# Kernel tuning notes

Hardware: AMD Instinct MI355X
Metric: run time of the kernel (lower is better)

Reference implementation:

```python
import jax, jax.numpy as jnp
import numpy as np

B, T, H = 2, 2048, 1024
NH, DK = 16, 64          # num_heads, head_dim (key)
VD, DV = 1024, 64        # value_dim, head_v_dim
LCTX, CD = 512, 768      # context length, cond_token_dim
DW, DA, DG, DVR = 64, 64, 128, 16  # lora ranks: decay, a, gate, v
EPS = DK * 1e-5          # GroupNorm eps = head_dim * norm_eps
LOGW_SCALE = -0.6065306597126334   # -exp(-0.5)

def _tshift(x):
    # token shift: out[t] = x[t-1], out[0] = 0
    return jnp.pad(x, ((0, 0), (1, 0), (0, 0)))[:, :-1]

def _forward(hidden_states, context, v_first, x_r, x_w, x_k, x_v, x_a, x_g,
             k_k, k_a, r_k, W_r, W_k, W_v, W_o, W_cond,
             wA, wB, wb, aA, aB, ab, gA, gB, vA, vB, vb, gn_w, gn_b):
    b, t, _ = hidden_states.shape
    # --- cross-attention context: project then linear-resample to length t (align_corners=True) ---
    ctx = context @ W_cond                                  # [B, Lctx, H]
    L = ctx.shape[1]
    pos = jnp.arange(t) * ((L - 1) / (t - 1))
    lo = jnp.floor(pos).astype(jnp.int32)
    hi = jnp.minimum(lo + 1, L - 1)
    f = (pos - lo)[None, :, None]
    ctx = ctx[:, lo] * (1.0 - f) + ctx[:, hi] * f            # [B, T, H]

    dx = _tshift(hidden_states) - hidden_states
    dc = _tshift(ctx) - ctx
    xr = hidden_states + dx * x_r
    xw = hidden_states + dx * x_w
    xa = hidden_states + dx * x_a
    xg = hidden_states + dx * x_g
    xk = ctx + dc * x_k   # key/value come from the (resampled) context: cross attention
    xv = ctx + dc * x_v

    r = xr @ W_r
    w = LOGW_SCALE * jax.nn.sigmoid(jnp.tanh(xw @ wA) @ wB + wb)   # log decay in (-0.6065, 0)
    k = xk @ W_k
    v = xv @ W_v
    # layer_idx != 0: lerp toward v_first with learned gate
    v = v + jax.nn.sigmoid((xv @ vA) @ vB + vb) * (v_first - v)
    a = jax.nn.sigmoid((xa @ aA) @ aB + ab)                         # in-context learning rate
    g = jax.nn.sigmoid(xg @ gA) @ gB                                 # output gate (no bias)

    kk = (k * k_k).reshape(b, t, NH, DK)
    kk = kk / jnp.maximum(jnp.linalg.norm(kk, axis=-1, keepdims=True), 1e-12)
    k = k * (1.0 + (a - 1.0) * k_a)

    rh = r.reshape(b, t, NH, DK)
    wh = w.reshape(b, t, NH, DK)
    kh = k.reshape(b, t, NH, DK)
    vh = v.reshape(b, t, NH, DV)
    ah = -kk
    bh = kk * a.reshape(b, t, NH, DK)

    # --- RWKV7 generalized delta rule recurrence: S[b,h,i(val),j(key)] ---
    def step(S, inp):
        r_t, w_t, k_t, v_t, a_t, b_t = inp
        sab = jnp.einsum('bhij,bhj,bhk->bhik', S, a_t, b_t)
        S = S * jnp.exp(w_t)[:, :, None, :] + sab + jnp.einsum('bhi,bhj->bhij', v_t, k_t)
        return S, jnp.einsum('bhij,bhj->bhi', S, r_t)

    tr = lambda x: jnp.swapaxes(x, 0, 1)  # [T,B,NH,D]
    S0 = jnp.zeros((b, NH, DV, DK), hidden_states.dtype)
    _, o = jax.lax.scan(step, S0, (tr(rh), tr(wh), tr(kh), tr(vh), tr(ah), tr(bh)))
    o = jnp.swapaxes(o, 0, 1)             # [B,T,NH,DV]

    # GroupNorm(num_groups=NH) over value_dim per token
    mu = o.mean(-1, keepdims=True)
    var = o.var(-1, keepdims=True)
    o = (o - mu) * jax.lax.rsqrt(var + EPS)
    o = o.reshape(b, t, VD) * gn_w + gn_b
    # r_k-weighted direct readout
    o = o + ((rh * kh * r_k).sum(-1, keepdims=True) * vh).reshape(b, t, VD)
    return (o * g) @ W_o

def setup_inputs():
    ki = iter(jax.random.split(jax.random.key(0), 48))
    def nrm(shape, s=1.0):
        return jax.random.normal(next(ki), shape, jnp.float32) * s
    def uni(shape):
        return jax.random.uniform(next(ki), shape, dtype=jnp.float32)
    return {
        'hidden_states': nrm((B, T, H)),
        'context': nrm((B, LCTX, CD)),
        'v_first': nrm((B, T, VD)),
        'x_r': uni((1, 1, H)), 'x_w': uni((1, 1, H)), 'x_k': uni((1, 1, H)),
        'x_v': uni((1, 1, H)), 'x_a': uni((1, 1, H)), 'x_g': uni((1, 1, H)),
        'k_k': jnp.full((H,), 0.85, jnp.float32),
        'k_a': jnp.ones((H,), jnp.float32),
        'r_k': nrm((NH, DK), 0.1),
        'W_r': nrm((H, H), 0.03), 'W_k': nrm((H, H), 0.03),
        'W_v': nrm((H, VD), 0.03), 'W_o': nrm((VD, H), 0.03),
        'W_cond': nrm((CD, H), 0.03),
        'wA': nrm((H, DW), 0.05), 'wB': nrm((DW, H), 0.05), 'wb': nrm((H,), 0.3) - 4.0,
        'aA': nrm((H, DA), 0.05), 'aB': nrm((DA, H), 0.05), 'ab': nrm((H,), 0.1),
        'gA': nrm((H, DG), 0.05), 'gB': nrm((DG, VD), 0.05),
        'vA': nrm((H, DVR), 0.05), 'vB': nrm((DVR, VD), 0.05),
        'vb': jnp.ones((VD,), jnp.float32),
        'gn_w': jnp.ones((VD,), jnp.float32), 'gn_b': jnp.zeros((VD,), jnp.float32),
    }

def reference(hidden_states, context, v_first, x_r, x_w, x_k, x_v, x_a, x_g, k_k, k_a, r_k, W_r, W_k, W_v, W_o, W_cond, wA, wB, wb, aA, aB, ab, gA, gB, vA, vB, vb, gn_w, gn_b):
    return _forward(hidden_states, context, v_first, x_r, x_w, x_k, x_v, x_a, x_g, k_k, k_a, r_k, W_r, W_k, W_v, W_o, W_cond, wA, wB, wb, aA, aB, ab, gA, gB, vA, vB, vb, gn_w, gn_b)
```

## Files before the change

kernel.cpp:

```cpp
#include <hip/hip_runtime.h>
#include <cstddef>
#include <cstdint>

#define T_ 2048
#define H_ 1024
#define NH_ 16
#define LCTX 512
#define NC 64
#define CL 32

typedef __attribute__((ext_vector_type(4))) float f4;
typedef __attribute__((ext_vector_type(4))) unsigned short u16x4;
typedef __attribute__((ext_vector_type(8))) short bf16x8;
typedef __attribute__((ext_vector_type(4))) float f32x4;

#define REP16(X) X(0) X(1) X(2) X(3) X(4) X(5) X(6) X(7) X(8) X(9) X(10) X(11) X(12) X(13) X(14) X(15)
#define REP8(X) X(0) X(1) X(2) X(3) X(4) X(5) X(6) X(7)
#define REP4(X) X(0) X(1) X(2) X(3)

__device__ __forceinline__ float sgm(float x) { return 1.0f / (1.0f + expf(-x)); }
__device__ __forceinline__ f4 f4splat(float v) { f4 r; r.x = v; r.y = v; r.z = v; r.w = v; return r; }
__device__ __forceinline__ float hsum4(f4 v) { return (v.x + v.y) + (v.z + v.w); }

__device__ __forceinline__ float rdlane(float v, int l) {
    return __uint_as_float(__builtin_amdgcn_readlane(__float_as_uint(v), l));
}

__device__ __forceinline__ unsigned short f2bf(float x) {
    unsigned u = __float_as_uint(x);
    u += 0x7FFFu + ((u >> 16) & 1u);
    return (unsigned short)(u >> 16);
}
__device__ __forceinline__ float bf2f(unsigned short h) {
    return __uint_as_float(((unsigned)h) << 16);
}

__device__ __forceinline__ void split1(float x, unsigned short& h, unsigned short& l) {
    unsigned u = __float_as_uint(x);
    h = (unsigned short)(u >> 16);
    float r = x - __uint_as_float(u & 0xFFFF0000u);
    l = (unsigned short)(__float_as_uint(r) >> 16);
}
__device__ __forceinline__ void split4(f4 v, u16x4& h, u16x4& l) {
    unsigned short hh, ll;
    split1(v.x, hh, ll); h.x = hh; l.x = ll;
    split1(v.y, hh, ll); h.y = hh; l.y = ll;
    split1(v.z, hh, ll); h.z = hh; l.z = ll;
    split1(v.w, hh, ll); h.w = hh; l.w = ll;
}

__device__ __forceinline__ size_t toff4(int row, int c4, int kpan) {
    const int j = c4 & 31;
    return ((size_t)(row >> 4) * kpan + (c4 >> 5)) * 512
         + ((j & 15) >> 2) * 128 + (row & 15) * 8 + ((j >> 4) << 2);
}
__device__ __forceinline__ size_t toff1(int row, int k, int kpan) {
    const int j = k & 31;
    return ((size_t)(row >> 4) * kpan + (k >> 5)) * 512
         + ((j & 15) >> 2) * 128 + (row & 15) * 8 + ((j >> 4) << 2) + (j & 3);
}

__device__ __forceinline__ void gload16(const void* g, void* l) {
    __builtin_amdgcn_global_load_lds(
        (const __attribute__((address_space(1))) unsigned int*)g,
        (__attribute__((address_space(3))) unsigned int*)l, 16, 0, 0);
}

struct WSeg { const float* W; unsigned short* Th; unsigned short* Tl;
              int K, N, kpan, tile0, tilesN; };
struct WAll { WSeg s[13]; };

__global__ __launch_bounds__(256) void wtrans_all(WAll all)
{
    const int bid = blockIdx.x;
    int si = 0;
    #pragma unroll
    for (int i = 1; i < 13; ++i) if (bid >= all.s[i].tile0) si = i;
    const WSeg sg = all.s[si];
    const int local = bid - sg.tile0;
    const int k0 = (local / sg.tilesN) * 32;
    const int n0 = (local % sg.tilesN) * 32;

    __shared__ float tile[32][33];
    const int t = threadIdx.x;
    const int r = t >> 3, c4 = (t & 7) * 4;
    f4 v = f4splat(0.0f);
    if (k0 + r < sg.K && n0 + c4 < sg.N)
        v = *(const f4*)(sg.W + (size_t)(k0 + r) * sg.N + n0 + c4);
    tile[r][c4 + 0] = v.x; tile[r][c4 + 1] = v.y;
    tile[r][c4 + 2] = v.z; tile[r][c4 + 3] = v.w;
    __syncthreads();
    {
        const int n = n0 + r;
        float x0 = tile[c4 + 0][r], x1 = tile[c4 + 1][r];
        float x2 = tile[c4 + 2][r], x3 = tile[c4 + 3][r];
        u16x4 hv, lv;
        hv.x = f2bf(x0); lv.x = f2bf(x0 - bf2f(hv.x));
        hv.y = f2bf(x1); lv.y = f2bf(x1 - bf2f(hv.y));
        hv.z = f2bf(x2); lv.z = f2bf(x2 - bf2f(hv.z));
        hv.w = f2bf(x3); lv.w = f2bf(x3 - bf2f(hv.w));
        const size_t off = toff4(n, k0 + c4, sg.kpan);
        *(u16x4*)(sg.Th + off) = hv;
        *(u16x4*)(sg.Tl + off) = lv;
    }
}

__global__ __launch_bounds__(256) void ctx_split(
    const float* __restrict__ X, unsigned short* __restrict__ H,
    unsigned short* __restrict__ L)
{
    const int gid = blockIdx.x * 256 + threadIdx.x;
    const int row = gid / 192;
    const int c4 = (gid - row * 192) * 4;
    f4 v = *(const f4*)(X + (size_t)row * 768 + c4);
    u16x4 h, l; split4(v, h, l);
    const size_t off = toff4(row, c4, 24);
    *(u16x4*)(H + off) = h; *(u16x4*)(L + off) = l;
}

__global__ __launch_bounds__(256) void hs_lerp4(
    const float* __restrict__ hs,
    const float* __restrict__ x_r, const float* __restrict__ x_w,
    const float* __restrict__ x_a, const float* __restrict__ x_g,
    unsigned short* __restrict__ xr_h, unsigned short* __restrict__ xr_l,
    unsigned short* __restrict__ xw_h, unsigned short* __restrict__ xw_l,
    unsigned short* __restrict__ xa_h, unsigned short* __restrict__ xa_l,
    unsigned short* __restrict__ xg_h, unsigned short* __restrict__ xg_l)
{
    const int gid = blockIdx.x * 256 + threadIdx.x;
    const int c4 = (gid & 255) * 4;
    const int row = gid >> 8;
    const int tt = row & (T_ - 1);
    const f4 cur = *(const f4*)(hs + (size_t)row * H_ + c4);
    f4 prev = f4splat(0.0f);
    if (tt) prev = *(const f4*)(hs + (size_t)(row - 1) * H_ + c4);
    const f4 d = prev - cur;
    const size_t off = toff4(row, c4, 32);
    u16x4 h, l;
    split4(cur + d * (*(const f4*)(x_r + c4)), h, l);
    *(u16x4*)(xr_h + off) = h; *(u16x4*)(xr_l + off) = l;
    split4(cur + d * (*(const f4*)(x_w + c4)), h, l);
    *(u16x4*)(xw_h + off) = h; *(u16x4*)(xw_l + off) = l;
    split4(cur + d * (*(const f4*)(x_a + c4)), h, l);
    *(u16x4*)(xa_h + off) = h; *(u16x4*)(xa_l + off) = l;
    split4(cur + d * (*(const f4*)(x_g + c4)), h, l);
    *(u16x4*)(xg_h + off) = h; *(u16x4*)(xg_l + off) = l;
}

__device__ __forceinline__ f4 ctx_sample(const float* __restrict__ cp, int b, int t, int c4) {
    const float scale = (float)(511.0 / 2047.0);
    float tf = (float)t * scale;
    int lo = (int)tf;
    float f = tf - (float)lo;
    int hi = lo + 1; if (hi > LCTX - 1) hi = LCTX - 1;
    f4 cl = *(const f4*)(cp + (size_t)(b * LCTX + lo) * 1024 + c4);
    f4 ch = *(const f4*)(cp + (size_t)(b * LCTX + hi) * 1024 + c4);
    return cl + (ch - cl) * f;
}

__global__ __launch_bounds__(256) void ctx_lerp2(
    const float* __restrict__ cp,
    const float* __restrict__ x_k, const float* __restrict__ x_v,
    unsigned short* __restrict__ xk_h, unsigned short* __restrict__ xk_l,
    unsigned short* __restrict__ xv_h, unsigned short* __restrict__ xv_l)
{
    const int gid = blockIdx.x * 256 + threadIdx.x;
    const int c4 = (gid & 255) * 4;
    const int row = gid >> 8;
    const int b = row >> 11;
    const int tt = row & (T_ - 1);
    const f4 cur = ctx_sample(cp, b, tt, c4);
    f4 prev = f4splat(0.0f);
    if (tt) prev = ctx_sample(cp, b, tt - 1, c4);
    const f4 d = prev - cur;
    const size_t off = toff4(row, c4, 32);
    u16x4 h, l;
    split4(cur + d * (*(const f4*)(x_k + c4)), h, l);
    *(u16x4*)(xk_h + off) = h; *(u16x4*)(xk_l + off) = l;
    split4(cur + d * (*(const f4*)(x_v + c4)), h, l);
    *(u16x4*)(xv_h + off) = h; *(u16x4*)(xv_l + off) = l;
}

struct GSeg {
    const unsigned short* ATh; const unsigned short* ATl;
    const unsigned short* BTh; const unsigned short* BTl;
    float* C; unsigned short* Ch; unsigned short* Cl;
    const float* bias; const float* aux1; const float* aux2;
    int K, N, kpanC, epi;
};
struct GBatch { GSeg s[4]; };

template <int OSPLIT>
__global__ __launch_bounds__(256, 2) void mgemm(GBatch gb, int M)
{
    __shared__ __align__(16) unsigned short Ah_[8 * 512];
    __shared__ __align__(16) unsigned short Al_[8 * 512];
    __shared__ __align__(16) unsigned short Bh_[4 * 512];
    __shared__ __align__(16) unsigned short Bl_[4 * 512];
    const GSeg G = gb.s[blockIdx.z];
    const int bn = blockIdx.y * 64;
    if (bn >= G.N) return;
    const int K = G.K;
    const int kpan = K >> 5;
    const int tid = threadIdx.x;
    const int lane = tid & 63;
    const int wave = tid >> 6;
    const int bm = blockIdx.x * 128;
    const int g = lane >> 4, rr = lane & 15;
    const int sA0 = wave, sA1 = wave + 4;

    f32x4 acc[4][2];
    #pragma unroll
    for (int mi = 0; mi < 4; ++mi)
        #pragma unroll
        for (int ni = 0; ni < 2; ++ni)
            acc[mi][ni] = (f32x4)(0.0f);

    const size_t aBase0 = (size_t)((bm >> 4) + sA0) * kpan * 512;
    const size_t aBase1 = (size_t)((bm >> 4) + sA1) * kpan * 512;
    const size_t bBase  = (size_t)((bn >> 4) + wave) * kpan * 512;

    for (int k0 = 0; k0 < K; k0 += 32) {
        const size_t kp = (size_t)(k0 >> 5) * 512 + (size_t)lane * 8;
        gload16(G.ATh + aBase0 + kp, &Ah_[sA0 * 512]);
        gload16(G.ATh + aBase1 + kp, &Ah_[sA1 * 512]);
        gload16(G.ATl + aBase0 + kp, &Al_[sA0 * 512]);
        gload16(G.ATl + aBase1 + kp, &Al_[sA1 * 512]);
        gload16(G.BTh + bBase + kp, &Bh_[wave * 512]);
        gload16(G.BTl + bBase + kp, &Bl_[wave * 512]);
        __syncthreads();
        bf16x8 a_h[4], a_l[4], b_h[2], b_l[2];
        #pragma unroll
        for (int mi = 0; mi < 4; ++mi) {
            const int s = (wave >> 1) * 4 + mi;
            a_h[mi] = *(const bf16x8*)&Ah_[s * 512 + g * 128 + rr * 8];
            a_l[mi] = *(const bf16x8*)&Al_[s * 512 + g * 128 + rr * 8];
        }
        #pragma unroll
        for (int ni = 0; ni < 2; ++ni) {
            const int s = (wave & 1) * 2 + ni;
            b_h[ni] = *(const bf16x8*)&Bh_[s * 512 + g * 128 + rr * 8];
            b_l[ni] = *(const bf16x8*)&Bl_[s * 512 + g * 128 + rr * 8];
        }
        #pragma unroll
        for (int mi = 0; mi < 4; ++mi)
            #pragma unroll
            for (int ni = 0; ni < 2; ++ni) {
                acc[mi][ni] = __builtin_amdgcn_mfma_f32_16x16x32_bf16(a_h[mi], b_h[ni], acc[mi][ni], 0, 0, 0);
                acc[mi][ni] = __builtin_amdgcn_mfma_f32_16x16x32_bf16(a_h[mi], b_l[ni], acc[mi][ni], 0, 0, 0);
                acc[mi][ni] = __builtin_amdgcn_mfma_f32_16x16x32_bf16(a_l[mi], b_h[ni], acc[mi][ni], 0, 0, 0);
            }
        __syncthreads();
    }
    const int wm = (wave >> 1) * 64;
    const int wn = (wave & 1) * 32;
    const int epi = G.epi;
    #pragma unroll
    for (int mi = 0; mi < 4; ++mi)
        #pragma unroll
        for (int ni = 0; ni < 2; ++ni)
            #pragma unroll
            for (int q = 0; q < 4; ++q) {
                const int grow = bm + wm + mi * 16 + g * 4 + q;
                const int gcol = bn + wn + ni * 16 + rr;
                float x = acc[mi][ni][q];
                if (epi == 1) x = -0.6065306597126334f * sgm(x + G.bias[gcol]);
                else if (epi == 2) x = sgm(x + G.bias[gcol]);
                else if (epi == 3) {
                    const size_t o3 = (size_t)grow * G.N + gcol;
                    float vt = G.aux1[o3];
                    x = vt + sgm(x + G.bias[gcol]) * (G.aux2[o3] - vt);
                }
                else if (epi == 4) x = tanhf(x);
                else if (epi == 5) x = sgm(x);
                if (OSPLIT) {
                    if (gcol < G.kpanC * 32) {
                        unsigned short hh, ll;
                        split1(x, hh, ll);
                        const size_t off = toff1(grow, gcol, G.kpanC);
                        G.Ch[off] = hh; G.Cl[off] = ll;
                    }
                } else {
                    G.C[(size_t)grow * G.N + gcol] = x;
                }
            }
}

__global__ __launch_bounds__(256) void prep_k(
    float* __restrict__ k, const float* __restrict__ a,
    const float* __restrict__ k_k, const float* __restrict__ k_a,
    float* __restrict__ kk)
{
    const int gid = blockIdx.x * 256 + threadIdx.x;
    const int j = gid & 63;
    const int h = (gid >> 6) & (NH_ - 1);
    const int ch = h * 64 + j;
    const float kv = k[gid];
    float kkv = kv * k_k[ch];
    float ss = kkv * kkv;
    #pragma unroll
    for (int m = 32; m; m >>= 1) ss += __shfl_xor(ss, m, 64);
    const float nrm = fmaxf(sqrtf(ss), 1e-12f);
    kk[gid] = kkv / nrm;
    const float av = a[gid];
    k[gid] = kv * (1.0f + (av - 1.0f) * k_a[ch]);
}

__global__ __launch_bounds__(256, 1) void chunk_AU(
    const float* __restrict__ w, const float* __restrict__ k,
    const float* __restrict__ v, const float* __restrict__ kk,
    const float* __restrict__ a,
    float* __restrict__ Pbuf, float* __restrict__ Ubuf)
{
    const int bid = blockIdx.x;
    const int c = bid & (NC - 1);
    const int bh = bid >> 6;
    const int b = bh >> 4, h = bh & (NH_ - 1);
    const int tid = threadIdx.x;
    const int wv_ = tid >> 6;
    const int half = wv_ & 1;
    const bool isU = wv_ >= 2;
    const int lane = tid & 63;
    __shared__ __align__(16) float ew_s[64], ah_s[64], bh_s[64], kh_s[64], vh_s[64];
    __shared__ float part[4][64];

#define DECL_X(i) f4 x##i = f4splat(0.0f);
    REP8(DECL_X)
#undef DECL_X
    if (!isU) {
        const int local = lane - half * 32;
#define INIT_Q(i) \
        if (local == 4*i+0) x##i.x = 1.0f; \
        else if (local == 4*i+1) x##i.y = 1.0f; \
        else if (local == 4*i+2) x##i.z = 1.0f; \
        else if (local == 4*i+3) x##i.w = 1.0f;
        REP8(INIT_Q)
#undef INIT_Q
    }

    size_t idx = (((size_t)b * T_ + (size_t)c * CL) * NH_ + h) * 64 + lane;
    float wvv = 0, kkv = 0, av = 0, kv = 0, vvv = 0;
    if (wv_ == 0) { wvv = w[idx]; kkv = kk[idx]; av = a[idx]; }
    else if (wv_ == 1) { kv = k[idx]; vvv = v[idx]; }

    for (int t = 0; t < CL; ++t) {
        if (wv_ == 0) {
            ew_s[lane] = expf(wvv);
            ah_s[lane] = -kkv;
            bh_s[lane] = kkv * av;
        } else if (wv_ == 1) {
            kh_s[lane] = kv;
            vh_s[lane] = vvv;
        }
        __syncthreads();
        if (t + 1 < CL) {
            idx += NH_ * 64;
            if (wv_ == 0) { wvv = w[idx]; kkv = kk[idx]; av = a[idx]; }
            else if (wv_ == 1) { kv = k[idx]; vvv = v[idx]; }
        }
        const f4* A4 = (const f4*)ah_s + half * 8;
        f4 da = f4splat(0.0f);
#define DOT_(i) { da += x##i * A4[i]; }
        REP8(DOT_)
#undef DOT_
        part[wv_][lane] = hsum4(da);
        __syncthreads();
        const float D = isU ? part[2][lane] + part[3][lane]
                            : part[0][lane] + part[1][lane];
        const float vcur = vh_s[lane];
        const f4* E4 = (const f4*)ew_s + half * 8;
        const f4* B4 = (const f4*)bh_s + half * 8;
        const f4* K4 = (const f4*)kh_s + half * 8;
        if (!isU) {
#define UPDQ_(i) { x##i = x##i * E4[i] + D * B4[i]; }
            REP8(UPDQ_)
#undef UPDQ_
        } else {
#define UPDU_(i) { x##i = x##i * E4[i] + D * B4[i] + vcur * K4[i]; }
            REP8(UPDU_)
#undef UPDU_
        }
        __syncthreads();
    }
    float* Dst = (isU ? Ubuf : Pbuf)
               + (((size_t)bh * NC + c) * 64 + lane) * 64 + half * 32;
#define ST_(i) ((f4*)Dst)[i] = x##i;
    REP8(ST_)
#undef ST_
}

__global__ __launch_bounds__(64) void chunk_scan(
    const float* __restrict__ Pbuf, float* __restrict__ USbuf)
{
    const int wg = (blockIdx.x & 7) * 64 + (blockIdx.x >> 3);
    const int bh = wg >> 4;
    const int rg = wg & 15;
    const int j = threadIdx.x;
    const int r0 = rg * 4;

    float a0 = 0, a1 = 0, a2 = 0, a3 = 0;
    float u0, u1, u2, u3;
    float pA[64], pB[64];

    const size_t base = (size_t)bh * NC * 4096;
    {
        const float* Pb = Pbuf + base + j;
        #pragma unroll
        for (int k2 = 0; k2 < 64; ++k2) pA[k2] = Pb[k2 * 64];
        const float* Ub = USbuf + base + r0 * 64 + j;
        u0 = Ub[0]; u1 = Ub[64]; u2 = Ub[128]; u3 = Ub[192];
    }

#define SCAN_STEP(PC, PN, c) { \
    float n0 = u0, n1 = u1, n2 = u2, n3 = u3; \
    float* Ub = USbuf + base + (size_t)(c) * 4096 + r0 * 64 + j; \
    Ub[0] = a0; Ub[64] = a1; Ub[128] = a2; Ub[192] = a3; \
    if ((c) + 1 < NC) { \
        const float* Un = USbuf + base + (size_t)((c) + 1) * 4096 + r0 * 64 + j; \
        u0 = Un[0]; u1 = Un[64]; u2 = Un[128]; u3 = Un[192]; \
        const float* Pn = Pbuf + base + (size_t)((c) + 1) * 4096 + j; \
        _Pragma("unroll") \
        for (int k2 = 0; k2 < 64; ++k2) PN[k2] = Pn[k2 * 64]; \
    } \
    _Pragma("unroll") \
    for (int k2 = 0; k2 < 64; ++k2) { \
        const float s0 = rdlane(a0, k2), s1 = rdlane(a1, k2); \
        const float s2 = rdlane(a2, k2), s3 = rdlane(a3, k2); \
        n0 += s0 * PC[k2]; n1 += s1 * PC[k2]; \
        n2 += s2 * PC[k2]; n3 += s3 * PC[k2]; \
    } \
    a0 = n0; a1 = n1; a2 = n2; a3 = n3; }

    for (int c = 0; c < NC; c += 2) {
        SCAN_STEP(pA, pB, c)
        SCAN_STEP(pB, pA, c + 1)
    }
#undef SCAN_STEP
}

__global__ __launch_bounds__(256, 1) void chunk_out(
    const float* __restrict__ r, const float* __restrict__ w,
    const float* __restrict__ k, const float* __restrict__ v,
    const float* __restrict__ kk, const float* __restrict__ a,
    const float* __restrict__ Scbuf, float* __restrict__ o)
{
    const int bid = blockIdx.x;
    const int c = bid & (NC - 1);
    const int bh = bid >> 6;
    const int b = bh >> 4, h = bh & (NH_ - 1);
    const int tid = threadIdx.x;
    const int wv_ = tid >> 6;
    const int lane = tid & 63;
    __shared__ __align__(16) float ew_s[64], ah_s[64], bh_s[64], kh_s[64], rh_s[64], vh_s[64];
    __shared__ float part[4][64];
    __shared__ float op_part[4][64];

#define DECL_S(i) f4 s##i;
    REP4(DECL_S)
#undef DECL_S
    const f4* Srow = (const f4*)(Scbuf + (((size_t)bh * NC + c) * 64 + lane) * 64 + wv_ * 16);
#define LD_S(i) s##i = Srow[i];
    REP4(LD_S)
#undef LD_S

    size_t idx = (((size_t)b * T_ + (size_t)c * CL) * NH_ + h) * 64 + lane;
    float wvv = 0, kkv = 0, av = 0, kv = 0, rv = 0, vvv = 0;
    if (wv_ == 0) { wvv = w[idx]; kkv = kk[idx]; av = a[idx]; }
    else if (wv_ == 1) { kv = k[idx]; rv = r[idx]; vvv = v[idx]; }

    float oprev = 0.0f;
    size_t oprev_idx = 0;

    for (int t = 0; t < CL; ++t) {
        if (t > 0 && wv_ == 0)
            o[oprev_idx] = oprev + op_part[1][lane] + op_part[2][lane] + op_part[3][lane];
        if (wv_ == 0) {
            ew_s[lane] = expf(wvv);
            ah_s[lane] = -kkv;
            bh_s[lane] = kkv * av;
        } else if (wv_ == 1) {
            kh_s[lane] = kv;
            rh_s[lane] = rv;
            vh_s[lane] = vvv;
        }
        const size_t oidx = idx;
        __syncthreads();
        if (t + 1 < CL) {
            idx += NH_ * 64;
            if (wv_ == 0) { wvv = w[idx]; kkv = kk[idx]; av = a[idx]; }
            else if (wv_ == 1) { kv = k[idx]; rv = r[idx]; vvv = v[idx]; }
        }
        const f4* A4 = (const f4*)ah_s + wv_ * 4;
        f4 ua = f4splat(0.0f);
#define DOTS_(i) { ua += s##i * A4[i]; }
        REP4(DOTS_)
#undef DOTS_
        part[wv_][lane] = hsum4(ua);
        __syncthreads();
        const float sa = (part[0][lane] + part[1][lane]) + (part[2][lane] + part[3][lane]);
        const float vcur = vh_s[lane];
        const f4* E4 = (const f4*)ew_s + wv_ * 4;
        const f4* B4 = (const f4*)bh_s + wv_ * 4;
        const f4* K4 = (const f4*)kh_s + wv_ * 4;
        const f4* R4 = (const f4*)rh_s + wv_ * 4;
        f4 oa = f4splat(0.0f);
#define UPDO_(i) { s##i = s##i * E4[i] + sa * B4[i] + vcur * K4[i]; oa += s##i * R4[i]; }
        REP4(UPDO_)
#undef UPDO_
        const float o_w = hsum4(oa);
        if (wv_ == 0) { oprev = o_w; oprev_idx = oidx; }
        else op_part[wv_][lane] = o_w;
        __syncthreads();
    }
    if (wv_ == 0)
        o[oprev_idx] = oprev + op_part[1][lane] + op_part[2][lane] + op_part[3][lane];
}

__global__ __launch_bounds__(256) void postproc(
    const float* __restrict__ o, const float* __restrict__ r, const float* __restrict__ k,
    const float* __restrict__ v, const float* __restrict__ g, const float* __restrict__ r_k,
    const float* __restrict__ gn_w, const float* __restrict__ gn_b,
    unsigned short* __restrict__ og_h, unsigned short* __restrict__ og_l)
{
    const int gid = blockIdx.x * 256 + threadIdx.x;
    const int i = gid & 63;
    const int h = (gid >> 6) & (NH_ - 1);
    const int ch = h * 64 + i;
    const float ov = o[gid];
    float s1 = ov, s2 = ov * ov;
    float term = r[gid] * k[gid] * r_k[ch];
    #pragma unroll
    for (int m = 32; m; m >>= 1) {
        s1 += __shfl_xor(s1, m, 64);
        s2 += __shfl_xor(s2, m, 64);
        term += __shfl_xor(term, m, 64);
    }
    const float mu = s1 * (1.0f / 64.0f);
    const float var = s2 * (1.0f / 64.0f) - mu * mu;
    const float on = (ov - mu) * rsqrtf(var + 6.4e-4f);
    const float outv = (on * gn_w[ch] + gn_b[ch] + term * v[gid]) * g[gid];
    unsigned short hh, ll;
    split1(outv, hh, ll);
    const int row = gid >> 10;
    const int col = gid & 1023;
    const size_t off = toff1(row, col, 32);
    og_h[off] = hh; og_l[off] = ll;
}

extern "C" void kernel_launch(void* const* d_in, const int* in_sizes, int n_in,
                              void* d_out, int out_size, void* d_ws, size_t ws_size,
                              hipStream_t stream)
{
    const float* hs      = (const float*)d_in[0];
    const float* context = (const float*)d_in[1];
    const float* v_first = (const float*)d_in[2];
    const float* x_r = (const float*)d_in[3];
    const float* x_w = (const float*)d_in[4];
    const float* x_k = (const float*)d_in[5];
    const float* x_v = (const float*)d_in[6];
    const float* x_a = (const float*)d_in[7];
    const float* x_g = (const float*)d_in[8];
    const float* k_k = (const float*)d_in[9];
    const float* k_a = (const float*)d_in[10];
    const float* r_k = (const float*)d_in[11];
    const float* W_r = (const float*)d_in[12];
    const float* W_k = (const float*)d_in[13];
    const float* W_v = (const float*)d_in[14];
    const float* W_o = (const float*)d_in[15];
    const float* W_cond = (const float*)d_in[16];
    const float* wA = (const float*)d_in[17];
    const float* wB = (const float*)d_in[18];
    const float* wb = (const float*)d_in[19];
    const float* aA = (const float*)d_in[20];
    const float* aB = (const float*)d_in[21];
    const float* ab = (const float*)d_in[22];
    const float* gA = (const float*)d_in[23];
    const float* gB = (const float*)d_in[24];
    const float* vA = (const float*)d_in[25];
    const float* vB = (const float*)d_in[26];
    const float* vb = (const float*)d_in[27];
    const float* gn_w = (const float*)d_in[28];
    const float* gn_b = (const float*)d_in[29];
    (void)in_sizes; (void)n_in; (void)out_size; (void)ws_size;

    float* ws = (float*)d_ws;
    float* cp    = ws;
    float* rbuf  = cp    + (1 << 20);
    float* kbuf  = rbuf  + (4 << 20);
    float* vtmp  = kbuf  + (4 << 20);
    float* wbuf  = vtmp  + (4 << 20);
    float* abuf  = wbuf  + (4 << 20);
    float* obuf  = abuf  + (4 << 20);
    float* kkbuf = obuf  + (4 << 20);
    float* gbuf  = kkbuf + (4 << 20);
    float* vbuf  = gbuf  + (4 << 20);
    float* Pbuf  = vbuf  + (4 << 20);
    float* Ubuf  = Pbuf  + (8 << 20);
    float* endf  = Ubuf  + (8 << 20);

    unsigned short* xr_h = (unsigned short*)obuf;  unsigned short* xr_l = xr_h + (4 << 20);
    unsigned short* xw_h = (unsigned short*)Pbuf;  unsigned short* xw_l = xw_h + (4 << 20);
    unsigned short* xa_h = (unsigned short*)Ubuf;  unsigned short* xa_l = xa_h + (4 << 20);
    unsigned short* xg_h = (unsigned short*)kkbuf; unsigned short* xg_l = xg_h + (4 << 20);
    unsigned short* xk_h = (unsigned short*)gbuf;  unsigned short* xk_l = xk_h + (4 << 20);
    unsigned short* xv_h = (unsigned short*)vbuf;  unsigned short* xv_l = xv_h + (4 << 20);
    unsigned short* og_h = (unsigned short*)wbuf;  unsigned short* og_l = og_h + (4 << 20);

    unsigned short* u = (unsigned short*)endf;
    unsigned short* ctx_h = u;  u += 786432;
    unsigned short* ctx_l = u;  u += 786432;
    unsigned short* w1h = u;    u += 262144;
    unsigned short* w1l = u;    u += 262144;
    unsigned short* a1h = u;    u += 262144;
    unsigned short* a1l = u;    u += 262144;
    unsigned short* g1h = u;    u += 524288;
    unsigned short* g1l = u;    u += 524288;
    unsigned short* v1h = u;    u += 131072;
    unsigned short* v1l = u;    u += 131072;
    unsigned short* condT_h = u; u += 786432;
    unsigned short* condT_l = u; u += 786432;
    unsigned short* rT_h = u;    u += 1048576;
    unsigned short* rT_l = u;    u += 1048576;
    unsigned short* kT_h = u;    u += 1048576;
    unsigned short* kT_l = u;    u += 1048576;
    unsigned short* vT_h = u;    u += 1048576;
    unsigned short* vT_l = u;    u += 1048576;
    unsigned short* oT_h = u;    u += 1048576;
    unsigned short* oT_l = u;    u += 1048576;
    unsigned short* waT_h = u;   u += 65536;
    unsigned short* waT_l = u;   u += 65536;
    unsigned short* wbT_h = u;   u += 65536;
    unsigned short* wbT_l = u;   u += 65536;
    unsigned short* aaT_h = u;   u += 65536;
    unsigned short* aaT_l = u;   u += 65536;
    unsigned short* abT_h = u;   u += 65536;
    unsigned short* abT_l = u;   u += 65536;
    unsigned short* gaT_h = u;   u += 131072;
    unsigned short* gaT_l = u;   u += 131072;
    unsigned short* gbT_h = u;   u += 131072;
    unsigned short* gbT_l = u;   u += 131072;
    unsigned short* vaT_h = u;   u += 65536;
    unsigned short* vaT_l = u;   u += 65536;
    unsigned short* vbT_h = u;   u += 32768;
    unsigned short* vbT_l = u;   u += 32768;

    const dim3 blk(256);
    {
        WAll all;
        auto seg = [](const float* W, unsigned short* Th, unsigned short* Tl,
                      int K, int N, int Kpad, int Npad, int tile0) {
            WSeg s; s.W = W; s.Th = Th; s.Tl = Tl; s.K = K; s.N = N;
            s.kpan = Kpad / 32; s.tile0 = tile0; s.tilesN = Npad / 32; return s;
        };
        int t0 = 0;
        all.s[0]  = seg(W_cond, condT_h, condT_l, 768, 1024, 768, 1024, t0);  t0 += 24 * 32;
        all.s[1]  = seg(W_r, rT_h, rT_l, 1024, 1024, 1024, 1024, t0);         t0 += 32 * 32;
        all.s[2]  = seg(W_k, kT_h, kT_l, 1024, 1024, 1024, 1024, t0);         t0 += 32 * 32;
        all.s[3]  = seg(W_v, vT_h, vT_l, 1024, 1024, 1024, 1024, t0);         t0 += 32 * 32;
        all.s[4]  = seg(W_o, oT_h, oT_l, 1024, 1024, 1024, 1024, t0);         t0 += 32 * 32;
        all.s[5]  = seg(wA, waT_h, waT_l, 1024, 64, 1024, 64, t0);            t0 += 32 * 2;
        all.s[6]  = seg(wB, wbT_h, wbT_l, 64, 1024, 64, 1024, t0);            t0 += 2 * 32;
        all.s[7]  = seg(aA, aaT_h, aaT_l, 1024, 64, 1024, 64, t0);            t0 += 32 * 2;
        all.s[8]  = seg(aB, abT_h, abT_l, 64, 1024, 64, 1024, t0);            t0 += 2 * 32;
        all.s[9]  = seg(gA, gaT_h, gaT_l, 1024, 128, 1024, 128, t0);          t0 += 32 * 4;
        all.s[10] = seg(gB, gbT_h, gbT_l, 128, 1024, 128, 1024, t0);          t0 += 4 * 32;
        all.s[11] = seg(vA, vaT_h, vaT_l, 1024, 16, 1024, 64, t0);            t0 += 32 * 2;
        all.s[12] = seg(vB, vbT_h, vbT_l, 16, 1024, 32, 1024, t0);            t0 += 1 * 32;
        wtrans_all<<<dim3(t0), blk, 0, stream>>>(all);
    }

    auto GS = [](const unsigned short* ah, const unsigned short* al,
                 const unsigned short* bh, const unsigned short* bl,
                 float* c, unsigned short* ch, unsigned short* cl,
                 int K, int N, int kpanC, int epi,
                 const float* bias, const float* a1, const float* a2) {
        GSeg s; s.ATh = ah; s.ATl = al; s.BTh = bh; s.BTl = bl;
        s.C = c; s.Ch = ch; s.Cl = cl; s.bias = bias; s.aux1 = a1; s.aux2 = a2;
        s.K = K; s.N = N; s.kpanC = kpanC; s.epi = epi; return s;
    };

    ctx_split<<<dim3(768), blk, 0, stream>>>(context, ctx_h, ctx_l);
    hs_lerp4<<<dim3(4096), blk, 0, stream>>>(hs, x_r, x_w, x_a, x_g,
                                             xr_h, xr_l, xw_h, xw_l, xa_h, xa_l, xg_h, xg_l);
    {
        GBatch gb;
        gb.s[0] = GS(ctx_h, ctx_l, condT_h, condT_l, cp, nullptr, nullptr,
                     768, 1024, 0, 0, nullptr, nullptr, nullptr);
        gb.s[1] = gb.s[0]; gb.s[2] = gb.s[0]; gb.s[3] = gb.s[0];
        mgemm<0><<<dim3(8, 16, 1), blk, 0, stream>>>(gb, 1024);
    }
    ctx_lerp2<<<dim3(4096), blk, 0, stream>>>(cp, x_k, x_v, xk_h, xk_l, xv_h, xv_l);

    {
        GBatch gb;
        gb.s[0] = GS(xr_h, xr_l, rT_h, rT_l, rbuf, nullptr, nullptr,
                     1024, 1024, 0, 0, nullptr, nullptr, nullptr);
        gb.s[1] = GS(xk_h, xk_l, kT_h, kT_l, kbuf, nullptr, nullptr,
                     1024, 1024, 0, 0, nullptr, nullptr, nullptr);
        gb.s[2] = GS(xv_h, xv_l, vT_h, vT_l, vtmp, nullptr, nullptr,
                     1024, 1024, 0, 0, nullptr, nullptr, nullptr);
        gb.s[3] = gb.s[0];
        mgemm<0><<<dim3(32, 16, 3), blk, 0, stream>>>(gb, 4096);
    }
    {
        GBatch gb;
        gb.s[0] = GS(xw_h, xw_l, waT_h, waT_l, nullptr, w1h, w1l,
                     1024, 64, 2, 4, nullptr, nullptr, nullptr);
        gb.s[1] = GS(xa_h, xa_l, aaT_h, aaT_l, nullptr, a1h, a1l,
                     1024, 64, 2, 0, nullptr, nullptr, nullptr);
        gb.s[2] = GS(xg_h, xg_l, gaT_h, gaT_l, nullptr, g1h, g1l,
                     1024, 128, 4, 5, nullptr, nullptr, nullptr);
        gb.s[3] = GS(xv_h, xv_l, vaT_h, vaT_l, nullptr, v1h, v1l,
                     1024, 64, 1, 0, nullptr, nullptr, nullptr);
        mgemm<1><<<dim3(32, 2, 4), blk, 0, stream>>>(gb, 4096);
    }
    {
        GBatch gb;
        gb.s[0] = GS(w1h, w1l, wbT_h, wbT_l, wbuf, nullptr, nullptr,
                     64, 1024, 0, 1, wb, nullptr, nullptr);
        gb.s[1] = GS(a1h, a1l, abT_h, abT_l, abuf, nullptr, nullptr,
                     64, 1024, 0, 2, ab, nullptr, nullptr);
        gb.s[2] = GS(g1h, g1l, gbT_h, gbT_l, gbuf, nullptr, nullptr,
                     128, 1024, 0, 0, nullptr, nullptr, nullptr);
        gb.s[3] = GS(v1h, v1l, vbT_h, vbT_l, vbuf, nullptr, nullptr,
                     32, 1024, 0, 3, vb, vtmp, v_first);
        mgemm<0><<<dim3(32, 16, 4), blk, 0, stream>>>(gb, 4096);
    }

    prep_k<<<dim3(16384), blk, 0, stream>>>(kbuf, abuf, k_k, k_a, kkbuf);
    chunk_AU<<<dim3(2048), dim3(256), 0, stream>>>(wbuf, kbuf, vbuf, kkbuf, abuf, Pbuf, Ubuf);
    chunk_scan<<<dim3(512), dim3(64), 0, stream>>>(Pbuf, Ubuf);
    chunk_out<<<dim3(2048), dim3(256), 0, stream>>>(rbuf, wbuf, kbuf, vbuf, kkbuf, abuf, Ubuf, obuf);

    postproc<<<dim3(16384), blk, 0, stream>>>(obuf, rbuf, kbuf, vbuf, gbuf, r_k, gn_w, gn_b, og_h, og_l);
    {
        GBatch gb;
        gb.s[0] = GS(og_h, og_l, oT_h, oT_l, (float*)d_out, nullptr, nullptr,
                     1024, 1024, 0, 0, nullptr, nullptr, nullptr);
        gb.s[1] = gb.s[0]; gb.s[2] = gb.s[0]; gb.s[3] = gb.s[0];
        mgemm<0><<<dim3(32, 16, 1), blk, 0, stream>>>(gb, 4096);
    }
}
```

Measured before the change: 628.4 us.

## Remap state rows to lane groups and double-buffer LDS in chunk kernels

In chunk_AU and chunk_out, each state row is now split across adjacent lanes (2 or 4) instead of across waves. The row dot-product reduction moves from LDS partial sums plus an extra barrier to intra-wave shuffles. The per-step inputs are double-buffered in shared memory, so each timestep needs one __syncthreads instead of two or three. The output is written directly by lane-group leaders. The cost is extra shuffles and a less coalesced access pattern for the scattered row state stores and loads.

```diff
diff --git a/kernel.cpp b/kernel.cpp
--- a/kernel.cpp
+++ b/kernel.cpp
@@ -318,17 +318,17 @@
     const int b = bh >> 4, h = bh & (NH_ - 1);
     const int tid = threadIdx.x;
     const int wv_ = tid >> 6;
-    const int half = wv_ & 1;
     const bool isU = wv_ >= 2;
     const int lane = tid & 63;
-    __shared__ __align__(16) float ew_s[64], ah_s[64], bh_s[64], kh_s[64], vh_s[64];
-    __shared__ float part[4][64];
+    const int row = (wv_ & 1) * 32 + (lane >> 1);
+    const int cb = (lane & 1) * 32;
+    __shared__ float ew_s[2][64], ah_s[2][64], bh_s[2][64], kh_s[2][64], vh_s[2][64];
 
 #define DECL_X(i) f4 x##i = f4splat(0.0f);
     REP8(DECL_X)
 #undef DECL_X
     if (!isU) {
-        const int local = lane - half * 32;
+        const int local = row - cb;
 #define INIT_Q(i) \
         if (local == 4*i+0) x##i.x = 1.0f; \
         else if (local == 4*i+1) x##i.y = 1.0f; \
@@ -342,35 +342,36 @@
     float wvv = 0, kkv = 0, av = 0, kv = 0, vvv = 0;
     if (wv_ == 0) { wvv = w[idx]; kkv = kk[idx]; av = a[idx]; }
     else if (wv_ == 1) { kv = k[idx]; vvv = v[idx]; }
+    if (wv_ == 0) { ew_s[0][lane] = expf(wvv); ah_s[0][lane] = -kkv; bh_s[0][lane] = kkv * av; }
+    else if (wv_ == 1) { kh_s[0][lane] = kv; vh_s[0][lane] = vvv; }
+    idx += NH_ * 64;
+    if (wv_ == 0) { wvv = w[idx]; kkv = kk[idx]; av = a[idx]; }
+    else if (wv_ == 1) { kv = k[idx]; vvv = v[idx]; }
+    __syncthreads();
 
     for (int t = 0; t < CL; ++t) {
-        if (wv_ == 0) {
-            ew_s[lane] = expf(wvv);
-            ah_s[lane] = -kkv;
-            bh_s[lane] = kkv * av;
-        } else if (wv_ == 1) {
-            kh_s[lane] = kv;
-            vh_s[lane] = vvv;
+        const int buf = t & 1;
+        if (t + 1 < CL) {
+            const int nb = buf ^ 1;
+            if (wv_ == 0) { ew_s[nb][lane] = expf(wvv); ah_s[nb][lane] = -kkv; bh_s[nb][lane] = kkv * av; }
+            else if (wv_ == 1) { kh_s[nb][lane] = kv; vh_s[nb][lane] = vvv; }
+            if (t + 2 < CL) {
+                idx += NH_ * 64;
+                if (wv_ == 0) { wvv = w[idx]; kkv = kk[idx]; av = a[idx]; }
+                else if (wv_ == 1) { kv = k[idx]; vvv = v[idx]; }
+            }
         }
-        __syncthreads();
-        if (t + 1 < CL) {
-            idx += NH_ * 64;
-            if (wv_ == 0) { wvv = w[idx]; kkv = kk[idx]; av = a[idx]; }
-            else if (wv_ == 1) { kv = k[idx]; vvv = v[idx]; }
-        }
-        const f4* A4 = (const f4*)ah_s + half * 8;
-        f4 da = f4splat(0.0f);
-#define DOT_(i) { da += x##i * A4[i]; }
-        REP8(DOT_)
-#undef DOT_
-        part[wv_][lane] = hsum4(da);
-        __syncthreads();
-        const float D = isU ? part[2][lane] + part[3][lane]
-                            : part[0][lane] + part[1][lane];
-        const float vcur = vh_s[lane];
-        const f4* E4 = (const f4*)ew_s + half * 8;
-        const f4* B4 = (const f4*)bh_s + half * 8;
-        const f4* K4 = (const f4*)kh_s + half * 8;
+        const f4* A4 = (const f4*)&ah_s[buf][cb];
+        f4 da0 = x0 * A4[0] + x2 * A4[2];
+        f4 da1 = x1 * A4[1] + x3 * A4[3];
+        da0 += x4 * A4[4] + x6 * A4[6];
+        da1 += x5 * A4[5] + x7 * A4[7];
+        const float Dp = hsum4(da0 + da1);
+        const float D = Dp + __shfl_xor(Dp, 1, 64);
+        const float vcur = vh_s[buf][row];
+        const f4* E4 = (const f4*)&ew_s[buf][cb];
+        const f4* B4 = (const f4*)&bh_s[buf][cb];
+        const f4* K4 = (const f4*)&kh_s[buf][cb];
         if (!isU) {
 #define UPDQ_(i) { x##i = x##i * E4[i] + D * B4[i]; }
             REP8(UPDQ_)
@@ -383,7 +384,7 @@
         __syncthreads();
     }
     float* Dst = (isU ? Ubuf : Pbuf)
-               + (((size_t)bh * NC + c) * 64 + lane) * 64 + half * 32;
+               + (((size_t)bh * NC + c) * 64 + row) * 64 + cb;
 #define ST_(i) ((f4*)Dst)[i] = x##i;
     REP8(ST_)
 #undef ST_
@@ -451,69 +452,69 @@
     const int tid = threadIdx.x;
     const int wv_ = tid >> 6;
     const int lane = tid & 63;
-    __shared__ __align__(16) float ew_s[64], ah_s[64], bh_s[64], kh_s[64], rh_s[64], vh_s[64];
-    __shared__ float part[4][64];
-    __shared__ float op_part[4][64];
+    const int row = wv_ * 16 + (lane >> 2);
+    const int cb = (lane & 3) * 16;
+    __shared__ float ew_s[2][64], ah_s[2][64], bh_s[2][64], kh_s[2][64], rh_s[2][64], vh_s[2][64];
 
 #define DECL_S(i) f4 s##i;
     REP4(DECL_S)
 #undef DECL_S
-    const f4* Srow = (const f4*)(Scbuf + (((size_t)bh * NC + c) * 64 + lane) * 64 + wv_ * 16);
+    const f4* Srow = (const f4*)(Scbuf + (((size_t)bh * NC + c) * 64 + row) * 64 + cb);
 #define LD_S(i) s##i = Srow[i];
     REP4(LD_S)
 #undef LD_S
 
     size_t idx = (((size_t)b * T_ + (size_t)c * CL) * NH_ + h) * 64 + lane;
+    size_t obase = (((size_t)b * T_ + (size_t)c * CL) * NH_ + h) * 64;
     float wvv = 0, kkv = 0, av = 0, kv = 0, rv = 0, vvv = 0;
     if (wv_ == 0) { wvv = w[idx]; kkv = kk[idx]; av = a[idx]; }
-    else if (wv_ == 1) { kv = k[idx]; rv = r[idx]; vvv = v[idx]; }
-
-    float oprev = 0.0f;
-    size_t oprev_idx = 0;
+    else if (wv_ == 1) { kv = k[idx]; rv = r[idx]; }
+    else if (wv_ == 2) { vvv = v[idx]; }
+    if (wv_ == 0) { ew_s[0][lane] = expf(wvv); ah_s[0][lane] = -kkv; bh_s[0][lane] = kkv * av; }
+    else if (wv_ == 1) { kh_s[0][lane] = kv; rh_s[0][lane] = rv; }
+    else if (wv_ == 2) { vh_s[0][lane] = vvv; }
+    idx += NH_ * 64;
+    if (wv_ == 0) { wvv = w[idx]; kkv = kk[idx]; av = a[idx]; }
+    else if (wv_ == 1) { kv = k[idx]; rv = r[idx]; }
+    else if (wv_ == 2) { vvv = v[idx]; }
+    __syncthreads();
 
     for (int t = 0; t < CL; ++t) {
-        if (t > 0 && wv_ == 0)
-            o[oprev_idx] = oprev + op_part[1][lane] + op_part[2][lane] + op_part[3][lane];
-        if (wv_ == 0) {
-            ew_s[lane] = expf(wvv);
-            ah_s[lane] = -kkv;
-            bh_s[lane] = kkv * av;
-        } else if (wv_ == 1) {
-            kh_s[lane] = kv;
-            rh_s[lane] = rv;
-            vh_s[lane] = vvv;
+        const int buf = t & 1;
+        if (t + 1 < CL) {
+            const int nb = buf ^ 1;
+            if (wv_ == 0) { ew_s[nb][lane] = expf(wvv); ah_s[nb][lane] = -kkv; bh_s[nb][lane] = kkv * av; }
+            else if (wv_ == 1) { kh_s[nb][lane] = kv; rh_s[nb][lane] = rv; }
+            else if (wv_ == 2) { vh_s[nb][lane] = vvv; }
+            if (t + 2 < CL) {
+                idx += NH_ * 64;
+                if (wv_ == 0) { wvv = w[idx]; kkv = kk[idx]; av = a[idx]; }
+                else if (wv_ == 1) { kv = k[idx]; rv = r[idx]; }
+                else if (wv_ == 2) { vvv = v[idx]; }
+            }
         }
-        const size_t oidx = idx;
-        __syncthreads();
-        if (t + 1 < CL) {
-            idx += NH_ * 64;
-            if (wv_ == 0) { wvv = w[idx]; kkv = kk[idx]; av = a[idx]; }
-            else if (wv_ == 1) { kv = k[idx]; rv = r[idx]; vvv = v[idx]; }
-        }
-        const f4* A4 = (const f4*)ah_s + wv_ * 4;
-        f4 ua = f4splat(0.0f);
-#define DOTS_(i) { ua += s##i * A4[i]; }
-        REP4(DOTS_)
-#undef DOTS_
-        part[wv_][lane] = hsum4(ua);
-        __syncthreads();
-        const float sa = (part[0][lane] + part[1][lane]) + (part[2][lane] + part[3][lane]);
-        const float vcur = vh_s[lane];
-        const f4* E4 = (const f4*)ew_s + wv_ * 4;
-        const f4* B4 = (const f4*)bh_s + wv_ * 4;
-        const f4* K4 = (const f4*)kh_s + wv_ * 4;
-        const f4* R4 = (const f4*)rh_s + wv_ * 4;
+        const f4* A4 = (const f4*)&ah_s[buf][cb];
+        f4 ua = (s0 * A4[0] + s1 * A4[1]) + (s2 * A4[2] + s3 * A4[3]);
+        float p = hsum4(ua);
+        p += __shfl_xor(p, 1, 64);
+        p += __shfl_xor(p, 2, 64);
+        const float sa = p;
+        const float vcur = vh_s[buf][row];
+        const f4* E4 = (const f4*)&ew_s[buf][cb];
+        const f4* B4 = (const f4*)&bh_s[buf][cb];
+        const f4* K4 = (const f4*)&kh_s[buf][cb];
+        const f4* R4 = (const f4*)&rh_s[buf][cb];
         f4 oa = f4splat(0.0f);
 #define UPDO_(i) { s##i = s##i * E4[i] + sa * B4[i] + vcur * K4[i]; oa += s##i * R4[i]; }
         REP4(UPDO_)
 #undef UPDO_
-        const float o_w = hsum4(oa);
-        if (wv_ == 0) { oprev = o_w; oprev_idx = oidx; }
-        else op_part[wv_][lane] = o_w;
+        float ow = hsum4(oa);
+        ow += __shfl_xor(ow, 1, 64);
+        ow += __shfl_xor(ow, 2, 64);
+        if ((lane & 3) == 0) o[obase + row] = ow;
+        obase += NH_ * 64;
         __syncthreads();
     }
-    if (wv_ == 0)
-        o[oprev_idx] = oprev + op_part[1][lane] + op_part[2][lane] + op_part[3][lane];
 }
 
 __global__ __launch_bounds__(256) void postproc(
```

Measured after the change: 635.9 us. Within noise of the previous version (+1.2%).

## Fuse chunk output with GroupNorm postproc using one wave per chunk

Applied to the files above, without the earlier changes.

Rewrites chunk_out so that each 64-lane wave owns a full chunk, holding all 64 state columns in registers and broadcasting per-token values with readlane. The shared-memory exchanges and the three barriers per token go away. The GroupNorm, bonus term, gating and bf16 split from postproc are folded into the same loop, so the o buffer is no longer written and read back and one launch is removed. In exchange each thread holds 64 floats of state and does four times the per-lane arithmetic, with four independent waves per block and a quarter of the blocks.

```diff
diff --git a/kernel.cpp b/kernel.cpp
--- a/kernel.cpp
+++ b/kernel.cpp
@@ -14,9 +14,7 @@
 typedef __attribute__((ext_vector_type(8))) short bf16x8;
 typedef __attribute__((ext_vector_type(4))) float f32x4;
 
-#define REP16(X) X(0) X(1) X(2) X(3) X(4) X(5) X(6) X(7) X(8) X(9) X(10) X(11) X(12) X(13) X(14) X(15)
 #define REP8(X) X(0) X(1) X(2) X(3) X(4) X(5) X(6) X(7)
-#define REP4(X) X(0) X(1) X(2) X(3)
 
 __device__ __forceinline__ float sgm(float x) { return 1.0f / (1.0f + expf(-x)); }
 __device__ __forceinline__ f4 f4splat(float v) { f4 r; r.x = v; r.y = v; r.z = v; r.w = v; return r; }
@@ -438,113 +436,101 @@
 #undef SCAN_STEP
 }
 
-__global__ __launch_bounds__(256, 1) void chunk_out(
+__global__ __launch_bounds__(256) void chunk_out_fused(
     const float* __restrict__ r, const float* __restrict__ w,
     const float* __restrict__ k, const float* __restrict__ v,
     const float* __restrict__ kk, const float* __restrict__ a,
-    const float* __restrict__ Scbuf, float* __restrict__ o)
-{
-    const int bid = blockIdx.x;
-    const int c = bid & (NC - 1);
-    const int bh = bid >> 6;
+    const float* __restrict__ Scbuf, const float* __restrict__ g,
+    const float* __restrict__ r_k, const float* __restrict__ gn_w,
+    const float* __restrict__ gn_b,
+    unsigned short* __restrict__ og_h, unsigned short* __restrict__ og_l)
+{
+    const int gw = blockIdx.x * 4 + (threadIdx.x >> 6);
+    const int c = gw & (NC - 1);
+    const int bh = gw >> 6;
     const int b = bh >> 4, h = bh & (NH_ - 1);
-    const int tid = threadIdx.x;
-    const int wv_ = tid >> 6;
-    const int lane = tid & 63;
-    __shared__ __align__(16) float ew_s[64], ah_s[64], bh_s[64], kh_s[64], rh_s[64], vh_s[64];
-    __shared__ float part[4][64];
-    __shared__ float op_part[4][64];
-
-#define DECL_S(i) f4 s##i;
-    REP4(DECL_S)
-#undef DECL_S
-    const f4* Srow = (const f4*)(Scbuf + (((size_t)bh * NC + c) * 64 + lane) * 64 + wv_ * 16);
-#define LD_S(i) s##i = Srow[i];
-    REP4(LD_S)
-#undef LD_S
+    const int lane = threadIdx.x & 63;
+    const int ch = h * 64 + lane;
+    const float rk_c = r_k[ch];
+    const float gnw_c = gn_w[ch];
+    const float gnb_c = gn_b[ch];
+
+    float s[64];
+    {
+        const float* Srow = Scbuf + (((size_t)bh * NC + c) * 64 + lane) * 64;
+        #pragma unroll
+        for (int j = 0; j < 64; ++j) s[j] = Srow[j];
+    }
 
     size_t idx = (((size_t)b * T_ + (size_t)c * CL) * NH_ + h) * 64 + lane;
-    float wvv = 0, kkv = 0, av = 0, kv = 0, rv = 0, vvv = 0;
-    if (wv_ == 0) { wvv = w[idx]; kkv = kk[idx]; av = a[idx]; }
-    else if (wv_ == 1) { kv = k[idx]; rv = r[idx]; vvv = v[idx]; }
-
-    float oprev = 0.0f;
-    size_t oprev_idx = 0;
+    int rowTok = b * T_ + c * CL;
+    float wv = w[idx], kkv = kk[idx], av = a[idx], kv = k[idx], rv = r[idx],
+          vv = v[idx], gv = g[idx];
 
     for (int t = 0; t < CL; ++t) {
-        if (t > 0 && wv_ == 0)
-            o[oprev_idx] = oprev + op_part[1][lane] + op_part[2][lane] + op_part[3][lane];
-        if (wv_ == 0) {
-            ew_s[lane] = expf(wvv);
-            ah_s[lane] = -kkv;
-            bh_s[lane] = kkv * av;
-        } else if (wv_ == 1) {
-            kh_s[lane] = kv;
-            rh_s[lane] = rv;
-            vh_s[lane] = vvv;
-        }
-        const size_t oidx = idx;
-        __syncthreads();
+        const float e_own = expf(wv);
+        const float ah_own = -kkv;
+        const float bh_own = kkv * av;
+        const float k_own = kv;
+        const float r_own = rv;
+        const float v_own = vv;
+        const float g_own = gv;
         if (t + 1 < CL) {
             idx += NH_ * 64;
-            if (wv_ == 0) { wvv = w[idx]; kkv = kk[idx]; av = a[idx]; }
-            else if (wv_ == 1) { kv = k[idx]; rv = r[idx]; vvv = v[idx]; }
-        }
-        const f4* A4 = (const f4*)ah_s + wv_ * 4;
-        f4 ua = f4splat(0.0f);
-#define DOTS_(i) { ua += s##i * A4[i]; }
-        REP4(DOTS_)
-#undef DOTS_
-        part[wv_][lane] = hsum4(ua);
-        __syncthreads();
-        const float sa = (part[0][lane] + part[1][lane]) + (part[2][lane] + part[3][lane]);
-        const float vcur = vh_s[lane];
-        const f4* E4 = (const f4*)ew_s + wv_ * 4;
-        const f4* B4 = (const f4*)bh_s + wv_ * 4;
-        const f4* K4 = (const f4*)kh_s + wv_ * 4;
-        const f4* R4 = (const f4*)rh_s + wv_ * 4;
-        f4 oa = f4splat(0.0f);
-#define UPDO_(i) { s##i = s##i * E4[i] + sa * B4[i] + vcur * K4[i]; oa += s##i * R4[i]; }
-        REP4(UPDO_)
-#undef UPDO_
-        const float o_w = hsum4(oa);
-        if (wv_ == 0) { oprev = o_w; oprev_idx = oidx; }
-        else op_part[wv_][lane] = o_w;
-        __syncthreads();
-    }
-    if (wv_ == 0)
-        o[oprev_idx] = oprev + op_part[1][lane] + op_part[2][lane] + op_part[3][lane];
-}
-
-__global__ __launch_bounds__(256) void postproc(
-    const float* __restrict__ o, const float* __restrict__ r, const float* __restrict__ k,
-    const float* __restrict__ v, const float* __restrict__ g, const float* __restrict__ r_k,
-    const float* __restrict__ gn_w, const float* __restrict__ gn_b,
-    unsigned short* __restrict__ og_h, unsigned short* __restrict__ og_l)
-{
-    const int gid = blockIdx.x * 256 + threadIdx.x;
-    const int i = gid & 63;
-    const int h = (gid >> 6) & (NH_ - 1);
-    const int ch = h * 64 + i;
-    const float ov = o[gid];
-    float s1 = ov, s2 = ov * ov;
-    float term = r[gid] * k[gid] * r_k[ch];
-    #pragma unroll
-    for (int m = 32; m; m >>= 1) {
-        s1 += __shfl_xor(s1, m, 64);
-        s2 += __shfl_xor(s2, m, 64);
-        term += __shfl_xor(term, m, 64);
-    }
-    const float mu = s1 * (1.0f / 64.0f);
-    const float var = s2 * (1.0f / 64.0f) - mu * mu;
-    const float on = (ov - mu) * rsqrtf(var + 6.4e-4f);
-    const float outv = (on * gn_w[ch] + gn_b[ch] + term * v[gid]) * g[gid];
-    unsigned short hh, ll;
-    split1(outv, hh, ll);
-    const int row = gid >> 10;
-    const int col = gid & 1023;
-    const size_t off = toff1(row, col, 32);
-    og_h[off] = hh; og_l[off] = ll;
+            wv = w[idx]; kkv = kk[idx]; av = a[idx]; kv = k[idx]; rv = r[idx];
+            vv = v[idx]; gv = g[idx];
+        }
+        float d0 = 0, d1 = 0, d2 = 0, d3 = 0;
+        #pragma unroll
+        for (int j = 0; j < 64; j += 4) {
+            d0 += s[j]     * rdlane(ah_own, j);
+            d1 += s[j + 1] * rdlane(ah_own, j + 1);
+            d2 += s[j + 2] * rdlane(ah_own, j + 2);
+            d3 += s[j + 3] * rdlane(ah_own, j + 3);
+        }
+        const float sa = (d0 + d1) + (d2 + d3);
+        float o0 = 0, o1 = 0, o2 = 0, o3 = 0;
+        #pragma unroll
+        for (int j = 0; j < 64; j += 4) {
+            {
+                const float ej = rdlane(e_own, j), bj = rdlane(bh_own, j);
+                const float kj = rdlane(k_own, j), rj = rdlane(r_own, j);
+                s[j] = s[j] * ej + sa * bj + v_own * kj; o0 += s[j] * rj;
+            }
+            {
+                const float ej = rdlane(e_own, j + 1), bj = rdlane(bh_own, j + 1);
+                const float kj = rdlane(k_own, j + 1), rj = rdlane(r_own, j + 1);
+                s[j + 1] = s[j + 1] * ej + sa * bj + v_own * kj; o1 += s[j + 1] * rj;
+            }
+            {
+                const float ej = rdlane(e_own, j + 2), bj = rdlane(bh_own, j + 2);
+                const float kj = rdlane(k_own, j + 2), rj = rdlane(r_own, j + 2);
+                s[j + 2] = s[j + 2] * ej + sa * bj + v_own * kj; o2 += s[j + 2] * rj;
+            }
+            {
+                const float ej = rdlane(e_own, j + 3), bj = rdlane(bh_own, j + 3);
+                const float kj = rdlane(k_own, j + 3), rj = rdlane(r_own, j + 3);
+                s[j + 3] = s[j + 3] * ej + sa * bj + v_own * kj; o3 += s[j + 3] * rj;
+            }
+        }
+        const float ov = (o0 + o1) + (o2 + o3);
+        float s1r = ov, s2r = ov * ov, term = r_own * k_own * rk_c;
+        #pragma unroll
+        for (int m = 32; m; m >>= 1) {
+            s1r += __shfl_xor(s1r, m, 64);
+            s2r += __shfl_xor(s2r, m, 64);
+            term += __shfl_xor(term, m, 64);
+        }
+        const float mu = s1r * (1.0f / 64.0f);
+        const float var = s2r * (1.0f / 64.0f) - mu * mu;
+        const float on = (ov - mu) * rsqrtf(var + 6.4e-4f);
+        const float outv = (on * gnw_c + gnb_c + term * v_own) * g_own;
+        unsigned short hh, ll;
+        split1(outv, hh, ll);
+        const size_t off = toff1(rowTok, ch, 32);
+        og_h[off] = hh; og_l[off] = ll;
+        ++rowTok;
+    }
 }
 
 extern "C" void kernel_launch(void* const* d_in, const int* in_sizes, int n_in,
@@ -604,7 +590,7 @@
     unsigned short* xg_h = (unsigned short*)kkbuf; unsigned short* xg_l = xg_h + (4 << 20);
     unsigned short* xk_h = (unsigned short*)gbuf;  unsigned short* xk_l = xk_h + (4 << 20);
     unsigned short* xv_h = (unsigned short*)vbuf;  unsigned short* xv_l = xv_h + (4 << 20);
-    unsigned short* og_h = (unsigned short*)wbuf;  unsigned short* og_l = og_h + (4 << 20);
+    unsigned short* og_h = (unsigned short*)obuf;  unsigned short* og_l = og_h + (4 << 20);
 
     unsigned short* u = (unsigned short*)endf;
     unsigned short* ctx_h = u;  u += 786432;
@@ -730,9 +716,9 @@
     prep_k<<<dim3(16384), blk, 0, stream>>>(kbuf, abuf, k_k, k_a, kkbuf);
     chunk_AU<<<dim3(2048), dim3(256), 0, stream>>>(wbuf, kbuf, vbuf, kkbuf, abuf, Pbuf, Ubuf);
     chunk_scan<<<dim3(512), dim3(64), 0, stream>>>(Pbuf, Ubuf);
-    chunk_out<<<dim3(2048), dim3(256), 0, stream>>>(rbuf, wbuf, kbuf, vbuf, kkbuf, abuf, Ubuf, obuf);
-
-    postproc<<<dim3(16384), blk, 0, stream>>>(obuf, rbuf, kbuf, vbuf, gbuf, r_k, gn_w, gn_b, og_h, og_l);
+    chunk_out_fused<<<dim3(512), dim3(256), 0, stream>>>(rbuf, wbuf, kbuf, vbuf, kkbuf, abuf,
+                                                         Ubuf, gbuf, r_k, gn_w, gn_b, og_h, og_l);
+
     {
         GBatch gb;
         gb.s[0] = GS(og_h, og_l, oT_h, oT_l, (float*)d_out, nullptr, nullptr,
```

New measurement: 622.4 us. No clear change (-1.0%).
